# Kernel tuning notes

Measured on AMD Instinct MI355X. Metric: run time of the kernel, lower is better.

The kernel has to match this reference:

```python
import jax, jax.numpy as jnp
import numpy as np

EPS = 1e-7  # keras.backend.epsilon()
ROUTINGS = 3


def squash(v, axis=-1):
    s2 = jnp.sum(jnp.square(v), axis=axis, keepdims=True)
    scale = s2 / (1.0 + s2) / jnp.sqrt(s2 + EPS)
    return scale * v


def setup_inputs() -> dict:
    key = jax.random.key(0)
    k1, k2 = jax.random.split(key)
    inputs = jax.random.normal(k1, (64, 2048, 16), dtype=jnp.float32)
    # glorot-style scale for W [J, K, Di, Do]
    W = jax.random.normal(k2, (2048, 32, 16, 32), dtype=jnp.float32) * (1.0 / np.sqrt(16 + 32))
    return {"inputs": inputs, "W": W}


def reference(inputs, W):
    # inputs: [B, J, Di], W: [J, K, Di, Do]
    inputs_hat = jnp.einsum('bji,jkio->bkjo', inputs, W)  # [B, K, J, Do]
    B = inputs.shape[0]
    K, J = W.shape[1], W.shape[0]
    b = jnp.zeros((B, K, J), dtype=inputs_hat.dtype)
    v = None
    for i in range(ROUTINGS):
        c = jax.nn.softmax(b, axis=1)                      # softmax over output capsules K
        s = jnp.einsum('bkj,bkjo->bko', c, inputs_hat)     # [B, K, Do]
        v = squash(s)
        if i < ROUTINGS - 1:
            b = b + jnp.einsum('bko,bkjo->bkj', v, inputs_hat)
    return v
```

## Files before the change

### kernel.cpp

```cpp
#include <hip/hip_runtime.h>
#include <hip/hip_bf16.h>

#define BB  64
#define JJ  2048
#define DI  16
#define KC  32
#define DOO 32
#define NKO 1024

typedef __bf16 bf16;
typedef __attribute__((ext_vector_type(8)))  __bf16 bf16x8;
typedef __attribute__((ext_vector_type(4)))  __bf16 bf16x4;
typedef __attribute__((ext_vector_type(4)))  float  f32x4;
typedef __attribute__((ext_vector_type(16))) float  f32x16;


__global__ __launch_bounds__(256)
void prep_x3(const float* __restrict__ X, bf16* __restrict__ Xfrag)
{
    int flat = blockIdx.x * 256 + threadIdx.x;
    int lane = flat & 63;
    int c01  = (flat >> 6) & 1;
    int j    = flat >> 7;
    int b    = c01 * 32 + (lane & 31);
    int i0   = (lane >> 5) * 8;
    const float* src = X + ((size_t)b * JJ + j) * DI + i0;
    bf16x8 o8;
#pragma unroll
    for (int e = 0; e < 8; ++e) o8[e] = (bf16)src[e];
    *reinterpret_cast<bf16x8*>(Xfrag + (size_t)flat * 8) = o8;
}

__device__ __forceinline__ void decode_qjr(int id, int& q, int& jr)
{
    q = (id >> 3) & 3; jr = ((id >> 5) << 3) | (id & 7);
}
__device__ __forceinline__ void decode_q8(int id, int& q8, int& jr)
{
    q8 = (id >> 3) & 7; jr = ((id >> 6) << 3) | (id & 7);
}
__device__ __forceinline__ int decode_jg(int id)
{
    return (id & 7) * 128 + (id >> 3);
}

__global__ __launch_bounds__(512, 6)
void caps_init8(const bf16* __restrict__ Xfrag, const float* __restrict__ Wg,
                bf16* __restrict__ Wfrag, bf16* __restrict__ partial, int Jc)
{
    const int tid  = threadIdx.x;
    const int w    = tid >> 6;
    const int lane = tid & 63;
    const int o31  = lane & 31;
    const int hi   = lane >> 5;
    int q8, jr; decode_q8(blockIdx.x, q8, jr);
    const int unit = q8 * 8 + w;
    const int k    = unit & 31;
    const int c01  = unit >> 5;

    f32x16 acc = {};

    const int j0 = jr * Jc;
    int jend = j0 + Jc; if (jend > JJ) jend = JJ;

    int j = j0;
    for (; j + 1 < jend; j += 2) {
        const float* ws0 = Wg + (size_t)j * 16384 + (size_t)k * 512 + hi * 256 + o31;
        const float* ws1 = ws0 + 16384;
        float a0[8], a1[8];
#pragma unroll
        for (int e = 0; e < 8; ++e) a0[e] = ws0[e * 32];
#pragma unroll
        for (int e = 0; e < 8; ++e) a1[e] = ws1[e * 32];
        bf16x8 fw0, fw1;
#pragma unroll
        for (int e = 0; e < 8; ++e) { fw0[e] = (bf16)a0[e]; fw1[e] = (bf16)a1[e]; }
        if (c01 == 0) {
            *reinterpret_cast<bf16x8*>(Wfrag + (((size_t)j * 32 + k) * 64 + lane) * 8)       = fw0;
            *reinterpret_cast<bf16x8*>(Wfrag + (((size_t)(j + 1) * 32 + k) * 64 + lane) * 8) = fw1;
        }
        bf16x8 fx0 = *reinterpret_cast<const bf16x8*>(Xfrag + (((size_t)j * 2 + c01) * 64 + lane) * 8);
        bf16x8 fx1 = *reinterpret_cast<const bf16x8*>(Xfrag + (((size_t)(j + 1) * 2 + c01) * 64 + lane) * 8);
        acc = __builtin_amdgcn_mfma_f32_32x32x16_bf16(fw0, fx0, acc, 0, 0, 0);
        acc = __builtin_amdgcn_mfma_f32_32x32x16_bf16(fw1, fx1, acc, 0, 0, 0);
    }
    for (; j < jend; ++j) {
        const float* ws = Wg + (size_t)j * 16384 + (size_t)k * 512 + hi * 256 + o31;
        bf16x8 fw;
#pragma unroll
        for (int e = 0; e < 8; ++e) fw[e] = (bf16)ws[e * 32];
        if (c01 == 0)
            *reinterpret_cast<bf16x8*>(Wfrag + (((size_t)j * 32 + k) * 64 + lane) * 8) = fw;
        bf16x8 fx = *reinterpret_cast<const bf16x8*>(Xfrag + (((size_t)j * 2 + c01) * 64 + lane) * 8);
        acc = __builtin_amdgcn_mfma_f32_32x32x16_bf16(fw, fx, acc, 0, 0, 0);
    }

    bf16* pout = partial + (size_t)jr * (BB * NKO);
#pragma unroll
    for (int qq = 0; qq < 4; ++qq) {
        bf16x4 o4;
#pragma unroll
        for (int rr = 0; rr < 4; ++rr) o4[rr] = (bf16)(acc[qq * 4 + rr] * 0.03125f);
        *reinterpret_cast<bf16x4*>(pout + (((size_t)unit * 4 + qq) * 64 + lane) * 4) = o4;
    }
}

__global__ __launch_bounds__(512, 6)
void caps_accum2(const bf16* __restrict__ Xfrag, const bf16* __restrict__ Wfrag,
                 const float* __restrict__ cbuf, bf16* __restrict__ partial, int Jc)
{
    const int tid  = threadIdx.x;
    const int w    = tid >> 6;
    const int lane = tid & 63;
    const int o31  = lane & 31;
    int q8, jr; decode_q8(blockIdx.x, q8, jr);
    const int unit = q8 * 8 + w;
    const int k    = unit & 31;
    const int c01  = unit >> 5;
    const int b    = c01 * 32 + o31;

    const f32x16 ZV16 = {};
    f32x16 acc = ZV16;

    const int j0 = jr * Jc;
    int jend = j0 + Jc; if (jend > JJ) jend = JJ;

    auto ldx = [&](int j) {
        return *reinterpret_cast<const bf16x8*>(Xfrag + (((size_t)j * 2 + c01) * 64 + lane) * 8);
    };
    auto ldw = [&](int j) {
        return *reinterpret_cast<const bf16x8*>(Wfrag + (((size_t)j * 32 + k) * 64 + lane) * 8);
    };
    auto ldc = [&](int j) {
        return cbuf[((size_t)j * 32 + k) * 64 + b];
    };

    bf16x8 fx = ldx(j0), fw = ldw(j0);
    float  cw = ldc(j0);

    for (int j = j0; j < jend; ++j) {
        const int jn = (j + 1 < jend) ? j + 1 : j;
        bf16x8 nfx = ldx(jn);
        bf16x8 nfw = ldw(jn);
        float  ncw = ldc(jn);
        f32x16 h = __builtin_amdgcn_mfma_f32_32x32x16_bf16(fw, fx, ZV16, 0, 0, 0);
#pragma unroll
        for (int r = 0; r < 16; ++r) acc[r] += cw * h[r];
        fx = nfx; fw = nfw; cw = ncw;
    }

    bf16* pout = partial + (size_t)jr * (BB * NKO);
#pragma unroll
    for (int qq = 0; qq < 4; ++qq) {
        bf16x4 o4;
#pragma unroll
        for (int rr = 0; rr < 4; ++rr) o4[rr] = (bf16)(acc[qq * 4 + rr]);
        *reinterpret_cast<bf16x4*>(pout + (((size_t)unit * 4 + qq) * 64 + lane) * 4) = o4;
    }
}

__global__ __launch_bounds__(512, 6)
void caps_logits8(const bf16* __restrict__ Xfrag, const bf16* __restrict__ Wfrag,
                  const float* __restrict__ vsumT, float* __restrict__ cbuf)
{
    __shared__ float lex[2][2][32][32];

    const int tid  = threadIdx.x;
    const int wv   = tid >> 6;
    const int lane = tid & 63;
    const int b31  = lane & 31;
    const int hi   = lane >> 5;
    const int c01  = wv & 1;
    const int kh2  = wv >> 1;
    const int jg   = decode_jg(blockIdx.x);
    const int j0   = jg * 2;
    const int b    = c01 * 32 + b31;

    const f32x16 ZV16 = {};

    bf16x8 fx0 = *reinterpret_cast<const bf16x8*>(Xfrag + (((size_t)j0 * 2 + c01) * 64 + lane) * 8);
    bf16x8 fx1 = *reinterpret_cast<const bf16x8*>(Xfrag + (((size_t)(j0 + 1) * 2 + c01) * 64 + lane) * 8);

    float lk[2][8];
#pragma unroll
    for (int kk = 0; kk < 8; ++kk) {
        const int k = kh2 * 8 + kk;
        const float* vt = vsumT + (size_t)k * 2048 + hi * 256 + b;
        float v[16];
#pragma unroll
        for (int qq = 0; qq < 4; ++qq)
#pragma unroll
            for (int rr = 0; rr < 4; ++rr)
                v[qq * 4 + rr] = vt[qq * 512 + rr * 64];
        const bf16* wf = Wfrag + (((size_t)j0 * 32 + k) * 64 + lane) * 8;
        bf16x8 fwa = *reinterpret_cast<const bf16x8*>(wf);
        bf16x8 fwb = *reinterpret_cast<const bf16x8*>(wf + 16384);
        f32x16 h0 = __builtin_amdgcn_mfma_f32_32x32x16_bf16(fwa, fx0, ZV16, 0, 0, 0);
        float a0 = 0.f;
#pragma unroll
        for (int r = 0; r < 16; ++r) a0 += h0[r] * v[r];
        f32x16 h1 = __builtin_amdgcn_mfma_f32_32x32x16_bf16(fwb, fx1, ZV16, 0, 0, 0);
        float a1 = 0.f;
#pragma unroll
        for (int r = 0; r < 16; ++r) a1 += h1[r] * v[r];
        a0 += __shfl_xor(a0, 32, 64);
        a1 += __shfl_xor(a1, 32, 64);
        lk[0][kk] = a0; lk[1][kk] = a1;
    }

    if (hi == 0) {
#pragma unroll
        for (int jj = 0; jj < 2; ++jj)
#pragma unroll
            for (int kk = 0; kk < 8; ++kk)
                lex[c01][jj][kh2 * 8 + kk][b31] = lk[jj][kk];
    }
    __syncthreads();

#pragma unroll
    for (int jj = 0; jj < 2; ++jj) {
        float mx = lex[c01][jj][0][b31];
#pragma unroll
        for (int k = 1; k < 32; ++k) mx = fmaxf(mx, lex[c01][jj][k][b31]);
        float sm = 0.f;
#pragma unroll
        for (int k = 0; k < 32; ++k) sm += __expf(lex[c01][jj][k][b31] - mx);
        float inv = 1.0f / sm;
#pragma unroll
        for (int kk = 0; kk < 8; ++kk)
            lk[jj][kk] = __expf(lk[jj][kk] - mx) * inv;
    }
    __syncthreads();

    if (hi == 0) {
#pragma unroll
        for (int jj = 0; jj < 2; ++jj)
#pragma unroll
            for (int kk = 0; kk < 8; ++kk)
                lex[c01][jj][kh2 * 8 + kk][b31] = lk[jj][kk];
    }
    __syncthreads();

    float* cj = cbuf + (size_t)j0 * 2048;
#pragma unroll
    for (int it = 0; it < 8; ++it) {
        int idx = it * 512 + tid;
        int b64 = idx & 63;
        int k   = (idx >> 6) & 31;
        int j2  = idx >> 11;
        cj[(size_t)j2 * 2048 + k * 64 + b64] = lex[b64 >> 5][j2][k][b64 & 31];
    }
}

__global__ __launch_bounds__(256)
void caps_red(const bf16* __restrict__ partial, float* __restrict__ vsum, float* __restrict__ vsumT,
              float* __restrict__ out, int P, int vmode, int wout)
{
    __shared__ float lds[4][32];
    const int unit = blockIdx.x;
    const int tid  = threadIdx.x;
    const int b31  = tid & 31;
    const int hi   = (tid >> 5) & 1;
    const int qq   = tid >> 6;
    const int k    = unit & 31;
    const int c01  = unit >> 5;

    const bf16* base = partial + (size_t)unit * 1024 + (size_t)tid * 4;
    f32x4 a = {};
    int p = 0;
    for (; p + 8 <= P; p += 8) {
        bf16x4 v[8];
#pragma unroll
        for (int u = 0; u < 8; ++u)
            v[u] = *reinterpret_cast<const bf16x4*>(base + (size_t)(p + u) * 65536);
#pragma unroll
        for (int u = 0; u < 8; ++u)
#pragma unroll
            for (int rr = 0; rr < 4; ++rr) a[rr] += (float)v[u][rr];
    }
    for (; p < P; ++p) {
        bf16x4 v = *reinterpret_cast<const bf16x4*>(base + (size_t)p * 65536);
#pragma unroll
        for (int rr = 0; rr < 4; ++rr) a[rr] += (float)v[rr];
    }

    float s2l = a[0] * a[0] + a[1] * a[1] + a[2] * a[2] + a[3] * a[3];
    s2l += __shfl_xor(s2l, 32, 64);
    if ((tid & 63) < 32) lds[qq][b31] = s2l;
    __syncthreads();
    float s2 = lds[0][b31] + lds[1][b31] + lds[2][b31] + lds[3][b31];
    float scale = s2 / (1.0f + s2) / sqrtf(s2 + 1e-7f);

    const int b  = c01 * 32 + b31;
    const int o0 = qq * 8 + hi * 4;
    size_t e0 = ((size_t)b * KC + k) * DOO + o0;
    float4 wv, nv;
    wv.x = scale * a[0]; wv.y = scale * a[1]; wv.z = scale * a[2]; wv.w = scale * a[3];
    if (vmode == 0) {
        nv = wv;
    } else if (vmode == 1) {
        float4 ov = *reinterpret_cast<const float4*>(vsum + e0);
        nv.x = ov.x + wv.x; nv.y = ov.y + wv.y; nv.z = ov.z + wv.z; nv.w = ov.w + wv.w;
    }
    if (vmode < 2) {
        *reinterpret_cast<float4*>(vsum + e0) = nv;
        vsumT[((size_t)k * 32 + o0 + 0) * 64 + b] = nv.x;
        vsumT[((size_t)k * 32 + o0 + 1) * 64 + b] = nv.y;
        vsumT[((size_t)k * 32 + o0 + 2) * 64 + b] = nv.z;
        vsumT[((size_t)k * 32 + o0 + 3) * 64 + b] = nv.w;
    }
    if (wout) *reinterpret_cast<float4*>(out + e0) = wv;
}

template<int UF, int MODE>
__global__ __launch_bounds__(1024, 8)
void caps_mm32(const bf16* __restrict__ Xfrag, const bf16* __restrict__ Wfrag,
               const float* __restrict__ Xf, const float* __restrict__ Wf,
               const float* __restrict__ cbuf, bf16* __restrict__ partial, int Jc)
{
    const int tid  = threadIdx.x;
    const int w    = tid >> 6;
    const int lane = tid & 63;
    const int o31  = lane & 31;
    const int hi   = lane >> 5;
    int q, jr; decode_qjr(blockIdx.x, q, jr);
    const int unit = q * 16 + w;
    const int k    = unit & 31;
    const int c01  = unit >> 5;
    const int b    = c01 * 32 + o31;

    const f32x16 ZV16 = {};
    f32x16 acc = ZV16;

    const int j0 = jr * Jc;
    int jend = j0 + Jc; if (jend > JJ) jend = JJ;

    for (int j = j0; j < jend; ++j) {
        bf16x8 fx, fw;
        if constexpr (UF) {
            fx = *reinterpret_cast<const bf16x8*>(Xfrag + (((size_t)j * 2 + c01) * 64 + lane) * 8);
            fw = *reinterpret_cast<const bf16x8*>(Wfrag + (((size_t)j * 32 + k) * 64 + lane) * 8);
        } else {
            const float* xs = Xf + ((size_t)b * JJ + j) * DI + hi * 8;
#pragma unroll
            for (int e = 0; e < 8; ++e) fx[e] = (bf16)xs[e];
            const float* ws = Wf + (size_t)j * 16384 + (size_t)k * 512 + hi * 256 + o31;
#pragma unroll
            for (int e = 0; e < 8; ++e) fw[e] = (bf16)ws[e * 32];
        }
        if constexpr (MODE == 0) {
            acc = __builtin_amdgcn_mfma_f32_32x32x16_bf16(fw, fx, acc, 0, 0, 0);
        } else {
            float cw = cbuf[((size_t)j * 32 + k) * 64 + b];
            f32x16 h = __builtin_amdgcn_mfma_f32_32x32x16_bf16(fw, fx, ZV16, 0, 0, 0);
#pragma unroll
            for (int r = 0; r < 16; ++r) acc[r] += cw * h[r];
        }
    }

    const float esc = (MODE == 0) ? 0.03125f : 1.0f;
    bf16* pout = partial + (size_t)jr * (BB * NKO);
#pragma unroll
    for (int qq = 0; qq < 4; ++qq) {
        bf16x4 o4;
#pragma unroll
        for (int rr = 0; rr < 4; ++rr) o4[rr] = (bf16)(acc[qq * 4 + rr] * esc);
        *reinterpret_cast<bf16x4*>(pout + (((size_t)unit * 4 + qq) * 64 + lane) * 4) = o4;
    }
}

template<int UF>
__global__ __launch_bounds__(256, 6)
void caps_logits32(const bf16* __restrict__ Xfrag, const bf16* __restrict__ Wfrag,
                   const float* __restrict__ Xf, const float* __restrict__ Wf,
                   const float* __restrict__ vsum, float* __restrict__ cbuf)
{
    __shared__ float cl[2][64][33];

    const int tid  = threadIdx.x;
    const int w    = tid >> 6;
    const int lane = tid & 63;
    const int o31  = lane & 31;
    const int hi   = lane >> 5;
    const int jg   = decode_jg(blockIdx.x);
    const int j0   = jg * 2;
    const int jj   = w >> 1;
    const int c01  = w & 1;
    const int j    = j0 + jj;
    const int b    = c01 * 32 + o31;

    const f32x16 ZV16 = {};

    bf16x8 fx;
    if constexpr (UF) {
        fx = *reinterpret_cast<const bf16x8*>(Xfrag + (((size_t)j * 2 + c01) * 64 + lane) * 8);
    } else {
        const float* xs = Xf + ((size_t)b * JJ + j) * DI + hi * 8;
#pragma unroll
        for (int e = 0; e < 8; ++e) fx[e] = (bf16)xs[e];
    }

    const float* vb = vsum + (size_t)b * NKO + hi * 4;
    float lk[32];
#pragma unroll
    for (int k = 0; k < 32; ++k) {
        bf16x8 fw;
        if constexpr (UF) {
            fw = *reinterpret_cast<const bf16x8*>(Wfrag + (((size_t)j * 32 + k) * 64 + lane) * 8);
        } else {
            const float* ws = Wf + (size_t)j * 16384 + (size_t)k * 512 + hi * 256 + o31;
#pragma unroll
            for (int e = 0; e < 8; ++e) fw[e] = (bf16)ws[e * 32];
        }
        f32x16 h = __builtin_amdgcn_mfma_f32_32x32x16_bf16(fw, fx, ZV16, 0, 0, 0);
        float a = 0.f;
        const float* vk = vb + k * 32;
#pragma unroll
        for (int qq = 0; qq < 4; ++qq) {
            float4 v4 = *reinterpret_cast<const float4*>(vk + qq * 8);
            a += h[qq * 4 + 0] * v4.x + h[qq * 4 + 1] * v4.y
               + h[qq * 4 + 2] * v4.z + h[qq * 4 + 3] * v4.w;
        }
        a += __shfl_xor(a, 32, 64);
        lk[k] = a;
    }

    float mx = lk[0];
#pragma unroll
    for (int k = 1; k < 32; ++k) mx = fmaxf(mx, lk[k]);
    float sm = 0.f;
#pragma unroll
    for (int k = 0; k < 32; ++k) { lk[k] = __expf(lk[k] - mx); sm += lk[k]; }
    float inv = 1.0f / sm;

    if (hi == 0) {
#pragma unroll
        for (int k = 0; k < 32; ++k) cl[jj][b][k] = lk[k] * inv;
    }
    __syncthreads();

#pragma unroll
    for (int j2 = 0; j2 < 2; ++j2) {
#pragma unroll
        for (int i = 0; i < 8; ++i) {
            int idx = i * 256 + tid;
            int kk = idx >> 6, bb = idx & 63;
            cbuf[((size_t)(j0 + j2) * 32 + kk) * 64 + bb] = cl[j2][bb][kk];
        }
    }
}

extern "C" void kernel_launch(void* const* d_in, const int* in_sizes, int n_in,
                              void* d_out, int out_size, void* d_ws, size_t ws_size,
                              hipStream_t stream)
{
    const float* X  = (const float*)d_in[0];
    const float* Wg = (const float*)d_in[1];
    float* out = (float*)d_out;

    const size_t WFRAG_B = (size_t)JJ * 32 * 64 * 8 * 2;
    const size_t XFRAG_B = (size_t)JJ * 2 * 64 * 8 * 2;
    const size_t VS_B    = 65536ull * 4;
    const size_t VT_B    = 65536ull * 4;
    const size_t CB_B    = (size_t)BB * JJ * KC * 4;
    const size_t FIX_B   = VS_B + VT_B + CB_B;

    int P = 128;
    int useFrag = 1;
    bf16 *Wfrag = nullptr, *Xfrag = nullptr, *partial = nullptr;
    float *vsum = nullptr, *vsumT = nullptr, *cbuf = nullptr;

    char* p = (char*)d_ws;
    if (ws_size >= WFRAG_B + XFRAG_B + FIX_B + (size_t)P * 65536 * 2) {
        Wfrag = (bf16*)p;            p += WFRAG_B;
        Xfrag = (bf16*)p;            p += XFRAG_B;
    } else {
        useFrag = 0;
        size_t avail = (ws_size > FIX_B) ? (ws_size - FIX_B) / (65536 * 2) : 8;
        P = (int)(avail & ~7ull);
        if (P < 8) P = 8;
        if (P > 128) P = 128;
    }
    vsum    = (float*)p;  p += VS_B;
    vsumT   = (float*)p;  p += VT_B;
    cbuf    = (float*)p;  p += CB_B;
    partial = (bf16*)p;

    const int Jc = (JJ + P - 1) / P;

    if (useFrag) {
        prep_x3<<<dim3(1024), dim3(256), 0, stream>>>(X, Xfrag);

        caps_init8<<<dim3(8 * P), dim3(512), 0, stream>>>(Xfrag, Wg, Wfrag, partial, Jc);
        caps_red<<<dim3(64), dim3(256), 0, stream>>>(partial, vsum, vsumT, out, P, 0, 0);

        caps_logits8<<<dim3(1024), dim3(512), 0, stream>>>(Xfrag, Wfrag, vsumT, cbuf);
        caps_accum2<<<dim3(8 * P), dim3(512), 0, stream>>>(Xfrag, Wfrag, cbuf, partial, Jc);
        caps_red<<<dim3(64), dim3(256), 0, stream>>>(partial, vsum, vsumT, out, P, 1, 0);

        caps_logits8<<<dim3(1024), dim3(512), 0, stream>>>(Xfrag, Wfrag, vsumT, cbuf);
        caps_accum2<<<dim3(8 * P), dim3(512), 0, stream>>>(Xfrag, Wfrag, cbuf, partial, Jc);
        caps_red<<<dim3(64), dim3(256), 0, stream>>>(partial, vsum, vsumT, out, P, 2, 1);
    } else {
        caps_mm32<0,0><<<dim3(4 * P), dim3(1024), 0, stream>>>(Xfrag, Wfrag, X, Wg, cbuf, partial, Jc);
        caps_red<<<dim3(64), dim3(256), 0, stream>>>(partial, vsum, vsumT, out, P, 0, 0);

        caps_logits32<0><<<dim3(1024), dim3(256), 0, stream>>>(Xfrag, Wfrag, X, Wg, vsum, cbuf);
        caps_mm32<0,1><<<dim3(4 * P), dim3(1024), 0, stream>>>(Xfrag, Wfrag, X, Wg, cbuf, partial, Jc);
        caps_red<<<dim3(64), dim3(256), 0, stream>>>(partial, vsum, vsumT, out, P, 1, 0);

        caps_logits32<0><<<dim3(1024), dim3(256), 0, stream>>>(Xfrag, Wfrag, X, Wg, vsum, cbuf);
        caps_mm32<0,1><<<dim3(4 * P), dim3(1024), 0, stream>>>(Xfrag, Wfrag, X, Wg, cbuf, partial, Jc);
        caps_red<<<dim3(64), dim3(256), 0, stream>>>(partial, vsum, vsumT, out, P, 2, 1);
    }
}
```

Measured before the change: 162.0 us.

## Fuse routing logits, softmax and weighted accumulation into one kernel

Replaces the separate logits/softmax kernel and the c-weighted accumulation kernel with a single caps_fused kernel. Each 1024-thread block walks its j-range, computes the agreement logits for all 32 capsules, does the softmax over k in shared memory with one barrier per j, and immediately accumulates c*u_hat into registers. This removes the 16 MB cbuf write and read per routing iteration and one launch per iteration. The price is a block-wide barrier on every j step. The partition count P also doubles to 256, which raises the workspace needed for partials and adds work to the reduction kernel.

```diff
diff --git a/kernel.cpp b/kernel.cpp
--- a/kernel.cpp
+++ b/kernel.cpp
@@ -42,6 +42,11 @@
 __device__ __forceinline__ int decode_jg(int id)
 {
     return (id & 7) * 128 + (id >> 3);
+}
+__device__ __forceinline__ void decode_f2(int id, int& c01, int& jr)
+{
+    int xcd = id & 7; int m = id >> 3;
+    c01 = m & 1; jr = ((m >> 1) << 3) | xcd;
 }
 
 __global__ __launch_bounds__(512, 6)
@@ -105,150 +110,103 @@
     }
 }
 
-__global__ __launch_bounds__(512, 6)
-void caps_accum2(const bf16* __restrict__ Xfrag, const bf16* __restrict__ Wfrag,
-                 const float* __restrict__ cbuf, bf16* __restrict__ partial, int Jc)
-{
+__global__ __launch_bounds__(1024, 8)
+void caps_fused(const bf16* __restrict__ Xfrag, const bf16* __restrict__ Wfrag,
+                const float* __restrict__ vsumT, bf16* __restrict__ partial, int Jc)
+{
+    __shared__ float lex[2][32][32];
+
     const int tid  = threadIdx.x;
     const int w    = tid >> 6;
     const int lane = tid & 63;
-    const int o31  = lane & 31;
-    int q8, jr; decode_q8(blockIdx.x, q8, jr);
-    const int unit = q8 * 8 + w;
-    const int k    = unit & 31;
-    const int c01  = unit >> 5;
-    const int b    = c01 * 32 + o31;
+    const int b31  = lane & 31;
+    const int hi   = lane >> 5;
+    int c01, jr; decode_f2(blockIdx.x, c01, jr);
+    const int k0   = 2 * w;
+    const int k1   = 2 * w + 1;
+    const int b    = c01 * 32 + b31;
 
     const f32x16 ZV16 = {};
-    f32x16 acc = ZV16;
+    f32x16 acc0 = ZV16, acc1 = ZV16;
 
     const int j0 = jr * Jc;
     int jend = j0 + Jc; if (jend > JJ) jend = JJ;
 
-    auto ldx = [&](int j) {
-        return *reinterpret_cast<const bf16x8*>(Xfrag + (((size_t)j * 2 + c01) * 64 + lane) * 8);
-    };
-    auto ldw = [&](int j) {
-        return *reinterpret_cast<const bf16x8*>(Wfrag + (((size_t)j * 32 + k) * 64 + lane) * 8);
-    };
-    auto ldc = [&](int j) {
-        return cbuf[((size_t)j * 32 + k) * 64 + b];
-    };
-
-    bf16x8 fx = ldx(j0), fw = ldw(j0);
-    float  cw = ldc(j0);
+    const float* vt0 = vsumT + (size_t)k0 * 2048 + hi * 256 + b;
+    const float* vt1 = vsumT + (size_t)k1 * 2048 + hi * 256 + b;
 
     for (int j = j0; j < jend; ++j) {
-        const int jn = (j + 1 < jend) ? j + 1 : j;
-        bf16x8 nfx = ldx(jn);
-        bf16x8 nfw = ldw(jn);
-        float  ncw = ldc(jn);
-        f32x16 h = __builtin_amdgcn_mfma_f32_32x32x16_bf16(fw, fx, ZV16, 0, 0, 0);
-#pragma unroll
-        for (int r = 0; r < 16; ++r) acc[r] += cw * h[r];
-        fx = nfx; fw = nfw; cw = ncw;
+        const int pb = j & 1;
+
+        bf16x8 fx = *reinterpret_cast<const bf16x8*>(Xfrag + (((size_t)j * 2 + c01) * 64 + lane) * 8);
+        const bf16* wfp = Wfrag + (((size_t)j * 32 + k0) * 64 + lane) * 8;
+        bf16x8 fw0 = *reinterpret_cast<const bf16x8*>(wfp);
+        bf16x8 fw1 = *reinterpret_cast<const bf16x8*>(wfp + 512);
+
+        float a0, a1;
+        {
+            f32x16 h = __builtin_amdgcn_mfma_f32_32x32x16_bf16(fw0, fx, ZV16, 0, 0, 0);
+            a0 = 0.f;
+#pragma unroll
+            for (int qq = 0; qq < 4; ++qq)
+#pragma unroll
+                for (int rr = 0; rr < 4; ++rr)
+                    a0 += h[qq * 4 + rr] * vt0[qq * 512 + rr * 64];
+        }
+        {
+            f32x16 h = __builtin_amdgcn_mfma_f32_32x32x16_bf16(fw1, fx, ZV16, 0, 0, 0);
+            a1 = 0.f;
+#pragma unroll
+            for (int qq = 0; qq < 4; ++qq)
+#pragma unroll
+                for (int rr = 0; rr < 4; ++rr)
+                    a1 += h[qq * 4 + rr] * vt1[qq * 512 + rr * 64];
+        }
+        a0 += __shfl_xor(a0, 32, 64);
+        a1 += __shfl_xor(a1, 32, 64);
+        if (hi == 0) {
+            lex[pb][k0][b31] = a0;
+            lex[pb][k1][b31] = a1;
+        }
+        __syncthreads();
+
+        float mx = lex[pb][0][b31];
+#pragma unroll
+        for (int k = 1; k < 32; ++k) mx = fmaxf(mx, lex[pb][k][b31]);
+        float sm = 0.f;
+#pragma unroll
+        for (int k = 0; k < 32; ++k) sm += __expf(lex[pb][k][b31] - mx);
+        float inv = 1.0f / sm;
+        float cw0 = __expf(a0 - mx) * inv;
+        float cw1 = __expf(a1 - mx) * inv;
+
+        {
+            f32x16 h = __builtin_amdgcn_mfma_f32_32x32x16_bf16(fw0, fx, ZV16, 0, 0, 0);
+#pragma unroll
+            for (int r = 0; r < 16; ++r) acc0[r] += cw0 * h[r];
+        }
+        {
+            f32x16 h = __builtin_amdgcn_mfma_f32_32x32x16_bf16(fw1, fx, ZV16, 0, 0, 0);
+#pragma unroll
+            for (int r = 0; r < 16; ++r) acc1[r] += cw1 * h[r];
+        }
     }
 
     bf16* pout = partial + (size_t)jr * (BB * NKO);
+    const int u0 = c01 * 32 + k0;
 #pragma unroll
     for (int qq = 0; qq < 4; ++qq) {
         bf16x4 o4;
 #pragma unroll
-        for (int rr = 0; rr < 4; ++rr) o4[rr] = (bf16)(acc[qq * 4 + rr]);
-        *reinterpret_cast<bf16x4*>(pout + (((size_t)unit * 4 + qq) * 64 + lane) * 4) = o4;
-    }
-}
-
-__global__ __launch_bounds__(512, 6)
-void caps_logits8(const bf16* __restrict__ Xfrag, const bf16* __restrict__ Wfrag,
-                  const float* __restrict__ vsumT, float* __restrict__ cbuf)
-{
-    __shared__ float lex[2][2][32][32];
-
-    const int tid  = threadIdx.x;
-    const int wv   = tid >> 6;
-    const int lane = tid & 63;
-    const int b31  = lane & 31;
-    const int hi   = lane >> 5;
-    const int c01  = wv & 1;
-    const int kh2  = wv >> 1;
-    const int jg   = decode_jg(blockIdx.x);
-    const int j0   = jg * 2;
-    const int b    = c01 * 32 + b31;
-
-    const f32x16 ZV16 = {};
-
-    bf16x8 fx0 = *reinterpret_cast<const bf16x8*>(Xfrag + (((size_t)j0 * 2 + c01) * 64 + lane) * 8);
-    bf16x8 fx1 = *reinterpret_cast<const bf16x8*>(Xfrag + (((size_t)(j0 + 1) * 2 + c01) * 64 + lane) * 8);
-
-    float lk[2][8];
-#pragma unroll
-    for (int kk = 0; kk < 8; ++kk) {
-        const int k = kh2 * 8 + kk;
-        const float* vt = vsumT + (size_t)k * 2048 + hi * 256 + b;
-        float v[16];
-#pragma unroll
-        for (int qq = 0; qq < 4; ++qq)
-#pragma unroll
-            for (int rr = 0; rr < 4; ++rr)
-                v[qq * 4 + rr] = vt[qq * 512 + rr * 64];
-        const bf16* wf = Wfrag + (((size_t)j0 * 32 + k) * 64 + lane) * 8;
-        bf16x8 fwa = *reinterpret_cast<const bf16x8*>(wf);
-        bf16x8 fwb = *reinterpret_cast<const bf16x8*>(wf + 16384);
-        f32x16 h0 = __builtin_amdgcn_mfma_f32_32x32x16_bf16(fwa, fx0, ZV16, 0, 0, 0);
-        float a0 = 0.f;
-#pragma unroll
-        for (int r = 0; r < 16; ++r) a0 += h0[r] * v[r];
-        f32x16 h1 = __builtin_amdgcn_mfma_f32_32x32x16_bf16(fwb, fx1, ZV16, 0, 0, 0);
-        float a1 = 0.f;
-#pragma unroll
-        for (int r = 0; r < 16; ++r) a1 += h1[r] * v[r];
-        a0 += __shfl_xor(a0, 32, 64);
-        a1 += __shfl_xor(a1, 32, 64);
-        lk[0][kk] = a0; lk[1][kk] = a1;
-    }
-
-    if (hi == 0) {
-#pragma unroll
-        for (int jj = 0; jj < 2; ++jj)
-#pragma unroll
-            for (int kk = 0; kk < 8; ++kk)
-                lex[c01][jj][kh2 * 8 + kk][b31] = lk[jj][kk];
-    }
-    __syncthreads();
-
-#pragma unroll
-    for (int jj = 0; jj < 2; ++jj) {
-        float mx = lex[c01][jj][0][b31];
-#pragma unroll
-        for (int k = 1; k < 32; ++k) mx = fmaxf(mx, lex[c01][jj][k][b31]);
-        float sm = 0.f;
-#pragma unroll
-        for (int k = 0; k < 32; ++k) sm += __expf(lex[c01][jj][k][b31] - mx);
-        float inv = 1.0f / sm;
-#pragma unroll
-        for (int kk = 0; kk < 8; ++kk)
-            lk[jj][kk] = __expf(lk[jj][kk] - mx) * inv;
-    }
-    __syncthreads();
-
-    if (hi == 0) {
-#pragma unroll
-        for (int jj = 0; jj < 2; ++jj)
-#pragma unroll
-            for (int kk = 0; kk < 8; ++kk)
-                lex[c01][jj][kh2 * 8 + kk][b31] = lk[jj][kk];
-    }
-    __syncthreads();
-
-    float* cj = cbuf + (size_t)j0 * 2048;
-#pragma unroll
-    for (int it = 0; it < 8; ++it) {
-        int idx = it * 512 + tid;
-        int b64 = idx & 63;
-        int k   = (idx >> 6) & 31;
-        int j2  = idx >> 11;
-        cj[(size_t)j2 * 2048 + k * 64 + b64] = lex[b64 >> 5][j2][k][b64 & 31];
+        for (int rr = 0; rr < 4; ++rr) o4[rr] = (bf16)acc0[qq * 4 + rr];
+        *reinterpret_cast<bf16x4*>(pout + (((size_t)u0 * 4 + qq) * 64 + lane) * 4) = o4;
+    }
+#pragma unroll
+    for (int qq = 0; qq < 4; ++qq) {
+        bf16x4 o4;
+#pragma unroll
+        for (int rr = 0; rr < 4; ++rr) o4[rr] = (bf16)acc1[qq * 4 + rr];
+        *reinterpret_cast<bf16x4*>(pout + (((size_t)(u0 + 1) * 4 + qq) * 64 + lane) * 4) = o4;
     }
 }
 
@@ -465,7 +423,7 @@
     const size_t CB_B    = (size_t)BB * JJ * KC * 4;
     const size_t FIX_B   = VS_B + VT_B + CB_B;
 
-    int P = 128;
+    int P = 256;
     int useFrag = 1;
     bf16 *Wfrag = nullptr, *Xfrag = nullptr, *partial = nullptr;
     float *vsum = nullptr, *vsumT = nullptr, *cbuf = nullptr;
@@ -494,12 +452,10 @@
         caps_init8<<<dim3(8 * P), dim3(512), 0, stream>>>(Xfrag, Wg, Wfrag, partial, Jc);
         caps_red<<<dim3(64), dim3(256), 0, stream>>>(partial, vsum, vsumT, out, P, 0, 0);
 
-        caps_logits8<<<dim3(1024), dim3(512), 0, stream>>>(Xfrag, Wfrag, vsumT, cbuf);
-        caps_accum2<<<dim3(8 * P), dim3(512), 0, stream>>>(Xfrag, Wfrag, cbuf, partial, Jc);
+        caps_fused<<<dim3(2 * P), dim3(1024), 0, stream>>>(Xfrag, Wfrag, vsumT, partial, Jc);
         caps_red<<<dim3(64), dim3(256), 0, stream>>>(partial, vsum, vsumT, out, P, 1, 0);
 
-        caps_logits8<<<dim3(1024), dim3(512), 0, stream>>>(Xfrag, Wfrag, vsumT, cbuf);
-        caps_accum2<<<dim3(8 * P), dim3(512), 0, stream>>>(Xfrag, Wfrag, cbuf, partial, Jc);
+        caps_fused<<<dim3(2 * P), dim3(1024), 0, stream>>>(Xfrag, Wfrag, vsumT, partial, Jc);
         caps_red<<<dim3(64), dim3(256), 0, stream>>>(partial, vsum, vsumT, out, P, 2, 1);
     } else {
         caps_mm32<0,0><<<dim3(4 * P), dim3(1024), 0, stream>>>(Xfrag, Wfrag, X, Wg, cbuf, partial, Jc);
```

Measured after the change: 517.9 us. 220% more time.
